# Kernel tuning notes

Hardware: AMD Instinct MI355X
Metric: run time of the kernel (lower is better)

## Reference

```python
import jax, jax.numpy as jnp
import numpy as np

N = 50000      # num nodes
E = 600000     # num edges (avg degree 12)
IN = 256       # in_feats
H = 128        # h_feats
P = 2          # prop_step
LN_EPS = 1e-5


def setup_inputs() -> dict:
    key = jax.random.key(0)
    ks = jax.random.split(key, 8)
    return {
        "in_feat": jax.random.normal(ks[0], (N, IN), jnp.float32),
        "row": jax.random.randint(ks[1], (E,), 0, N),  # target node of each edge
        "col": jax.random.randint(ks[2], (E,), 0, N),  # source node of each edge
        "lin_w": jax.random.normal(ks[3], (H, IN), jnp.float32) / np.sqrt(IN).astype(np.float32),
        "lin_b": jnp.zeros((H,), jnp.float32),
        "conv_w": jax.random.normal(ks[4], (H, H), jnp.float32) / np.sqrt(H).astype(np.float32),
        "conv_b": jnp.zeros((H,), jnp.float32),
        "root_emb": jax.random.normal(ks[5], (1, H), jnp.float32) * 0.02,
        "ln_gamma": jnp.ones((P, H), jnp.float32),
        "ln_beta": jnp.zeros((P, H), jnp.float32),
    }


def _layernorm(x, g, b):
    mu = jnp.mean(x, axis=-1, keepdims=True)
    var = jnp.mean(jnp.square(x - mu), axis=-1, keepdims=True)
    return (x - mu) * jax.lax.rsqrt(var + LN_EPS) * g + b


def reference(in_feat, row, col, lin_w, lin_b, conv_w, conv_b, root_emb, ln_gamma, ln_beta):
    n = in_feat.shape[0]
    h = in_feat @ lin_w.T + lin_b                      # [N, H]

    # OGB-style degree norm with +1 trick (original edges, row = target)
    deg = jax.ops.segment_sum(jnp.ones_like(row, dtype=h.dtype), row, num_segments=n) + 1.0
    deg_inv = 1.0 / deg                                # deg >= 1, never inf

    # GCNConv symmetric norm with self loops: D^-1/2 (A+I) D^-1/2
    loop = jnp.arange(n)
    r2 = jnp.concatenate([row, loop])                  # [E+N] targets
    c2 = jnp.concatenate([col, loop])                  # [E+N] sources
    d2 = jax.ops.segment_sum(jnp.ones_like(r2, dtype=h.dtype), r2, num_segments=n)
    dis = jnp.where(d2 > 0, jax.lax.rsqrt(jnp.maximum(d2, 1.0)), 0.0)
    ew = dis[r2] * dis[c2]                             # [E+N] edge weights

    root = root_emb[0]                                 # [H]
    ori = h
    for i in range(P):
        if i != 0:
            h = h + ori                                # residual
            h = _layernorm(h, ln_gamma[i], ln_beta[i])
            h = jax.nn.relu(h)
            # dropout=0.0 -> identity
        xw = h @ conv_w.T                              # [N, H]
        h_msg = jax.ops.segment_sum(ew[:, None] * xw[c2], r2, num_segments=n) + conv_b
        root_contrib = jax.nn.relu(h + root) * deg_inv[:, None]
        h = h_msg + root_contrib
    return h
```

## Files before the change

### kernel.cpp

```cpp
#include <hip/hip_runtime.h>

#define NN 50000
#define EE 600000
#define INF 256
#define HF 128
#define CEB ((EE + 255) / 256)

typedef __attribute__((ext_vector_type(8))) short short8;
typedef __attribute__((ext_vector_type(4))) float floatx4;

__device__ __forceinline__ unsigned short f32_to_bf16_rne(float x) {
    unsigned int u = __float_as_uint(x);
    unsigned int r = (u + 0x7FFFu + ((u >> 16) & 1u)) >> 16;
    return (unsigned short)r;
}
__device__ __forceinline__ float bf16_to_f32(unsigned short h) {
    return __uint_as_float(((unsigned int)h) << 16);
}
__device__ __forceinline__ float bf16lo_u32(unsigned int u) {
    return __uint_as_float(u << 16);
}
__device__ __forceinline__ float bf16hi_u32(unsigned int u) {
    return __uint_as_float(u & 0xFFFF0000u);
}
__device__ __forceinline__ void cvt_hilo8(float4 v0, float4 v1, short8& hs, short8& ls) {
    float x[8] = {v0.x, v0.y, v0.z, v0.w, v1.x, v1.y, v1.z, v1.w};
    union { short8 s; unsigned short u[8]; } H, L;
#pragma unroll
    for (int k = 0; k < 8; ++k) {
        unsigned short hi = f32_to_bf16_rne(x[k]);
        H.u[k] = hi;
        L.u[k] = f32_to_bf16_rne(x[k] - bf16_to_f32(hi));
    }
    hs = H.s;
    ls = L.s;
}

__global__ void count_and_prepack(const int* __restrict__ row, int* __restrict__ cnt,
                                  int* __restrict__ pos, int E,
                                  const float* __restrict__ lw, const float* __restrict__ cw,
                                  unsigned short* __restrict__ fl, unsigned short* __restrict__ fc) {
    int b = blockIdx.x;
    if (b < CEB) {
        int e = b * 256 + threadIdx.x;
        if (e < E) pos[e] = atomicAdd(&cnt[row[e]], 1);
        return;
    }
    int idx = (b - CEB) * 256 + threadIdx.x;
    const float* src;
    unsigned short* dst;
    int K, c;
    if (idx < 8192) {
        src = lw; dst = fl; K = INF; c = idx;
    } else if (idx < 12288) {
        src = cw; dst = fc; K = HF; c = idx - 8192;
    } else return;
    int lane = c & 63;
    int nt = (c >> 6) & 7;
    int hl = (c >> 9) & 1;
    int kc = c >> 10;
    int rw = nt * 16 + (lane & 15);
    int koff = kc * 32 + (lane >> 4) * 8;
    const float* p = &src[(size_t)rw * K + koff];
    float4 v0 = *reinterpret_cast<const float4*>(p);
    float4 v1 = *reinterpret_cast<const float4*>(p + 4);
    short8 hs, ls;
    cvt_hilo8(v0, v1, hs, ls);
    *reinterpret_cast<short8*>(&dst[(size_t)c * 8]) = hl ? ls : hs;
}

__global__ void scan_phase1(const int* __restrict__ cnt, int* __restrict__ bsum, int n) {
    __shared__ int sdata[256];
    int t = threadIdx.x;
    int i = blockIdx.x * 256 + t;
    sdata[t] = (i < n) ? cnt[i] : 0;
    __syncthreads();
    for (int s = 128; s > 0; s >>= 1) {
        if (t < s) sdata[t] += sdata[t + s];
        __syncthreads();
    }
    if (t == 0) bsum[blockIdx.x] = sdata[0];
}

__global__ void scan_phase3(const int* __restrict__ cnt, const int* __restrict__ bsum,
                            int* __restrict__ row_start,
                            float* __restrict__ deg_inv, float* __restrict__ dis,
                            int n, int nb, int E) {
    __shared__ int sb[256];
    __shared__ int sdata[256];
    int t = threadIdx.x;
    sb[t] = (t < nb) ? bsum[t] : 0;
    __syncthreads();
    for (int s = 1; s < 256; s <<= 1) {
        int add = (t >= s) ? sb[t - s] : 0;
        __syncthreads();
        sb[t] += add;
        __syncthreads();
    }
    int base = sb[blockIdx.x] - bsum[blockIdx.x];
    int i = blockIdx.x * 256 + t;
    int v = (i < n) ? cnt[i] : 0;
    sdata[t] = v;
    __syncthreads();
    for (int s = 1; s < 256; s <<= 1) {
        int add = (t >= s) ? sdata[t - s] : 0;
        __syncthreads();
        sdata[t] += add;
        __syncthreads();
    }
    if (i < n) {
        int ex = base + sdata[t] - v;
        row_start[i] = ex;
        float d = (float)(v + 1);
        deg_inv[i] = 1.0f / d;
        dis[i] = rsqrtf(d);
    }
    if (blockIdx.x == 0 && t == 0) row_start[n] = E;
}

__global__ void fill_csr(const int* __restrict__ row, const int* __restrict__ col,
                         const int* __restrict__ row_start, const int* __restrict__ pos,
                         int* __restrict__ csr_col, int E) {
    int e = blockIdx.x * blockDim.x + threadIdx.x;
    if (e < E) {
        int p = row_start[row[e]] + pos[e];
        __builtin_nontemporal_store(col[e], &csr_col[p]);
    }
}

template <int K, int MODE>
__global__ __launch_bounds__(256) void gemm_ldsw(
    const float* __restrict__ Af,
    const unsigned short* __restrict__ Ahg, const unsigned short* __restrict__ Alg,
    const unsigned short* __restrict__ Wf,
    const float* __restrict__ bias,
    float* __restrict__ C, unsigned short* __restrict__ Cbf,
    const float* __restrict__ h, const float* __restrict__ deg_inv,
    const float* __restrict__ dis, const float* __restrict__ root,
    const float* __restrict__ gamma, const float* __restrict__ beta,
    int M) {
    constexpr int NKC = K / 32;
    __shared__ unsigned short WS[2 * 8192];

    const int t = threadIdx.x;
    const int wave = t >> 6;
    const int lane = t & 63;
    const int lrow = lane & 15;
    const int quad = lane >> 4;
    const int bm = blockIdx.x * 64;
    int arow = bm + wave * 16 + lrow;
    if (arow >= M) arow = M - 1;

    floatx4 acc[8];
#pragma unroll
    for (int nt = 0; nt < 8; ++nt) acc[nt] = (floatx4){0.f, 0.f, 0.f, 0.f};

#pragma unroll
    for (int p = 0; p < NKC / 2; ++p) {
        if (p) __syncthreads();
        {
            const uint4* src = reinterpret_cast<const uint4*>(Wf + (size_t)p * 16384);
            uint4* dstl = reinterpret_cast<uint4*>(WS);
#pragma unroll
            for (int i = 0; i < 8; ++i) dstl[t + 256 * i] = src[t + 256 * i];
        }
        __syncthreads();
#pragma unroll
        for (int k2 = 0; k2 < 2; ++k2) {
            int kc = p * 2 + k2;
            short8 afh, afl;
            if (MODE == 0) {
                const float* ap = &Af[(size_t)arow * K + kc * 32 + quad * 8];
                float4 a0 = *reinterpret_cast<const float4*>(ap);
                float4 a1 = *reinterpret_cast<const float4*>(ap + 4);
                cvt_hilo8(a0, a1, afh, afl);
            } else {
                size_t ao = (size_t)arow * K + kc * 32 + quad * 8;
                afh = *reinterpret_cast<const short8*>(&Ahg[ao]);
                afl = *reinterpret_cast<const short8*>(&Alg[ao]);
            }
            const unsigned short* wb = &WS[k2 * 8192 + lane * 8];
#pragma unroll
            for (int nt = 0; nt < 8; ++nt) {
                short8 bfh = *reinterpret_cast<const short8*>(wb + nt * 512);
                short8 bfl = *reinterpret_cast<const short8*>(wb + 4096 + nt * 512);
                acc[nt] = __builtin_amdgcn_mfma_f32_16x16x32_bf16(afh, bfh, acc[nt], 0, 0, 0);
                acc[nt] = __builtin_amdgcn_mfma_f32_16x16x32_bf16(afl, bfh, acc[nt], 0, 0, 0);
                acc[nt] = __builtin_amdgcn_mfma_f32_16x16x32_bf16(afh, bfl, acc[nt], 0, 0, 0);
            }
        }
    }

    float cb[8], rt[8], gm[8], bt[8];
#pragma unroll
    for (int nt = 0; nt < 8; ++nt) {
        int colh = nt * 16 + lrow;
        cb[nt] = bias[colh];
        if (MODE >= 1) rt[nt] = root[colh];
        if (MODE == 1) { gm[nt] = gamma[colh]; bt[nt] = beta[colh]; }
    }

#pragma unroll
    for (int r = 0; r < 4; ++r) {
        int grow = bm + wave * 16 + quad * 4 + r;
        bool ok = (grow < M);
        int gr = ok ? grow : M - 1;
        float x[8];
        if (MODE == 0) {
#pragma unroll
            for (int nt = 0; nt < 8; ++nt) x[nt] = acc[nt][r] + cb[nt];
        } else {
            float di = deg_inv[gr];
            float hv[8];
#pragma unroll
            for (int nt = 0; nt < 8; ++nt) hv[nt] = h[(size_t)gr * HF + nt * 16 + lrow];
#pragma unroll
            for (int nt = 0; nt < 8; ++nt) {
                float v = acc[nt][r] + cb[nt] + fmaxf(hv[nt] + rt[nt], 0.f) * di;
                x[nt] = (MODE == 1) ? v + hv[nt] : v;
            }
        }
        if (MODE == 1) {
            float s = 0.f;
#pragma unroll
            for (int nt = 0; nt < 8; ++nt) s += x[nt];
#pragma unroll
            for (int m = 1; m < 16; m <<= 1) s += __shfl_xor(s, m, 64);
            float mu = s * (1.0f / HF);
            float var = 0.f;
#pragma unroll
            for (int nt = 0; nt < 8; ++nt) { float d = x[nt] - mu; var += d * d; }
#pragma unroll
            for (int m = 1; m < 16; m <<= 1) var += __shfl_xor(var, m, 64);
            float rs = rsqrtf(var * (1.0f / HF) + 1e-5f);
            float ds = dis[gr];
            if (ok) {
#pragma unroll
                for (int nt = 0; nt < 8; ++nt) {
                    int colh = nt * 16 + lrow;
                    float y = fmaxf((x[nt] - mu) * rs * gm[nt] + bt[nt], 0.f);
                    C[(size_t)grow * HF + colh] = y;
                    Cbf[(size_t)grow * HF + colh] = f32_to_bf16_rne(ds * y);
                }
            }
        } else if (MODE == 0) {
            if (ok) {
                float ds = dis[grow];
#pragma unroll
                for (int nt = 0; nt < 8; ++nt) {
                    int colh = nt * 16 + lrow;
                    C[(size_t)grow * HF + colh] = x[nt];
                    Cbf[(size_t)grow * HF + colh] = f32_to_bf16_rne(ds * x[nt]);
                }
            }
        } else {
            if (ok) {
#pragma unroll
                for (int nt = 0; nt < 8; ++nt)
                    C[(size_t)grow * HF + nt * 16 + lrow] = x[nt];
            }
        }
    }
}

__global__ void aggregate(const int* __restrict__ row_start, const int* __restrict__ csr_col,
                          const float* __restrict__ dis, const float* __restrict__ deg_inv,
                          const float* __restrict__ h, const unsigned short* __restrict__ hbf,
                          unsigned short* __restrict__ agg_hi, unsigned short* __restrict__ agg_lo,
                          int n) {
    int wid = (blockIdx.x * blockDim.x + threadIdx.x) >> 6;
    int lane = threadIdx.x & 63;
    if (wid >= n) return;
    int q = lane >> 4;
    int l16 = lane & 15;
    int s = row_start[wid];
    int e = row_start[wid + 1];
    float a0 = 0.f, a1 = 0.f, a2 = 0.f, a3 = 0.f, a4 = 0.f, a5 = 0.f, a6 = 0.f, a7 = 0.f;
    if (e - s <= 16) {
        int j0 = s + q;
        bool p0 = j0 < e, p1 = j0 + 4 < e, p2 = j0 + 8 < e, p3 = j0 + 12 < e;
        int c0 = p0 ? csr_col[j0] : 0;
        int c1 = p1 ? csr_col[j0 + 4] : 0;
        int c2 = p2 ? csr_col[j0 + 8] : 0;
        int c3 = p3 ? csr_col[j0 + 12] : 0;
        uint4 z = make_uint4(0, 0, 0, 0);
        uint4 g0 = z, g1 = z, g2 = z, g3 = z;
        if (p0) g0 = *reinterpret_cast<const uint4*>(&hbf[(size_t)c0 * HF + l16 * 8]);
        if (p1) g1 = *reinterpret_cast<const uint4*>(&hbf[(size_t)c1 * HF + l16 * 8]);
        if (p2) g2 = *reinterpret_cast<const uint4*>(&hbf[(size_t)c2 * HF + l16 * 8]);
        if (p3) g3 = *reinterpret_cast<const uint4*>(&hbf[(size_t)c3 * HF + l16 * 8]);
        a0 = bf16lo_u32(g0.x) + bf16lo_u32(g1.x) + bf16lo_u32(g2.x) + bf16lo_u32(g3.x);
        a1 = bf16hi_u32(g0.x) + bf16hi_u32(g1.x) + bf16hi_u32(g2.x) + bf16hi_u32(g3.x);
        a2 = bf16lo_u32(g0.y) + bf16lo_u32(g1.y) + bf16lo_u32(g2.y) + bf16lo_u32(g3.y);
        a3 = bf16hi_u32(g0.y) + bf16hi_u32(g1.y) + bf16hi_u32(g2.y) + bf16hi_u32(g3.y);
        a4 = bf16lo_u32(g0.z) + bf16lo_u32(g1.z) + bf16lo_u32(g2.z) + bf16lo_u32(g3.z);
        a5 = bf16hi_u32(g0.z) + bf16hi_u32(g1.z) + bf16hi_u32(g2.z) + bf16hi_u32(g3.z);
        a6 = bf16lo_u32(g0.w) + bf16lo_u32(g1.w) + bf16lo_u32(g2.w) + bf16lo_u32(g3.w);
        a7 = bf16hi_u32(g0.w) + bf16hi_u32(g1.w) + bf16hi_u32(g2.w) + bf16hi_u32(g3.w);
    } else {
        float b0 = 0.f, b1 = 0.f, b2 = 0.f, b3 = 0.f, b4 = 0.f, b5 = 0.f, b6 = 0.f, b7 = 0.f;
        int j = s + q;
        for (; j + 4 < e; j += 8) {
            int c0 = csr_col[j];
            int c1 = csr_col[j + 4];
            uint4 h0 = *reinterpret_cast<const uint4*>(&hbf[(size_t)c0 * HF + l16 * 8]);
            uint4 h1 = *reinterpret_cast<const uint4*>(&hbf[(size_t)c1 * HF + l16 * 8]);
            a0 += bf16lo_u32(h0.x); a1 += bf16hi_u32(h0.x);
            a2 += bf16lo_u32(h0.y); a3 += bf16hi_u32(h0.y);
            a4 += bf16lo_u32(h0.z); a5 += bf16hi_u32(h0.z);
            a6 += bf16lo_u32(h0.w); a7 += bf16hi_u32(h0.w);
            b0 += bf16lo_u32(h1.x); b1 += bf16hi_u32(h1.x);
            b2 += bf16lo_u32(h1.y); b3 += bf16hi_u32(h1.y);
            b4 += bf16lo_u32(h1.z); b5 += bf16hi_u32(h1.z);
            b6 += bf16lo_u32(h1.w); b7 += bf16hi_u32(h1.w);
        }
        if (j < e) {
            int c0 = csr_col[j];
            uint4 h0 = *reinterpret_cast<const uint4*>(&hbf[(size_t)c0 * HF + l16 * 8]);
            a0 += bf16lo_u32(h0.x); a1 += bf16hi_u32(h0.x);
            a2 += bf16lo_u32(h0.y); a3 += bf16hi_u32(h0.y);
            a4 += bf16lo_u32(h0.z); a5 += bf16hi_u32(h0.z);
            a6 += bf16lo_u32(h0.w); a7 += bf16hi_u32(h0.w);
        }
        a0 += b0; a1 += b1; a2 += b2; a3 += b3;
        a4 += b4; a5 += b5; a6 += b6; a7 += b7;
    }
#pragma unroll
    for (int m = 16; m < 64; m <<= 1) {
        a0 += __shfl_xor(a0, m, 64);
        a1 += __shfl_xor(a1, m, 64);
        a2 += __shfl_xor(a2, m, 64);
        a3 += __shfl_xor(a3, m, 64);
        a4 += __shfl_xor(a4, m, 64);
        a5 += __shfl_xor(a5, m, 64);
        a6 += __shfl_xor(a6, m, 64);
        a7 += __shfl_xor(a7, m, 64);
    }
    if (q == 0) {
        float dn = dis[wid];
        float di = deg_inv[wid];
        float4 hA = *reinterpret_cast<const float4*>(&h[(size_t)wid * HF + l16 * 8]);
        float4 hB = *reinterpret_cast<const float4*>(&h[(size_t)wid * HF + l16 * 8 + 4]);
        float o[8];
        o[0] = fmaf(dn, a0, di * hA.x);
        o[1] = fmaf(dn, a1, di * hA.y);
        o[2] = fmaf(dn, a2, di * hA.z);
        o[3] = fmaf(dn, a3, di * hA.w);
        o[4] = fmaf(dn, a4, di * hB.x);
        o[5] = fmaf(dn, a5, di * hB.y);
        o[6] = fmaf(dn, a6, di * hB.z);
        o[7] = fmaf(dn, a7, di * hB.w);
        unsigned short hi[8], lo[8];
#pragma unroll
        for (int k = 0; k < 8; ++k) {
            hi[k] = f32_to_bf16_rne(o[k]);
            lo[k] = f32_to_bf16_rne(o[k] - bf16_to_f32(hi[k]));
        }
        uint4 hp, lp;
        hp.x = (unsigned)hi[0] | ((unsigned)hi[1] << 16);
        hp.y = (unsigned)hi[2] | ((unsigned)hi[3] << 16);
        hp.z = (unsigned)hi[4] | ((unsigned)hi[5] << 16);
        hp.w = (unsigned)hi[6] | ((unsigned)hi[7] << 16);
        lp.x = (unsigned)lo[0] | ((unsigned)lo[1] << 16);
        lp.y = (unsigned)lo[2] | ((unsigned)lo[3] << 16);
        lp.z = (unsigned)lo[4] | ((unsigned)lo[5] << 16);
        lp.w = (unsigned)lo[6] | ((unsigned)lo[7] << 16);
        *reinterpret_cast<uint4*>(&agg_hi[(size_t)wid * HF + l16 * 8]) = hp;
        *reinterpret_cast<uint4*>(&agg_lo[(size_t)wid * HF + l16 * 8]) = lp;
    }
}

extern "C" void kernel_launch(void* const* d_in, const int* in_sizes, int n_in,
                              void* d_out, int out_size, void* d_ws, size_t ws_size,
                              hipStream_t stream) {
    const int N = NN, E = EE;
    const float* in_feat = (const float*)d_in[0];
    const int* row = (const int*)d_in[1];
    const int* col = (const int*)d_in[2];
    const float* lin_w = (const float*)d_in[3];
    const float* lin_b = (const float*)d_in[4];
    const float* conv_w = (const float*)d_in[5];
    const float* conv_b = (const float*)d_in[6];
    const float* root_emb = (const float*)d_in[7];
    const float* ln_gamma = (const float*)d_in[8];
    const float* ln_beta = (const float*)d_in[9];
    float* out = (float*)d_out;

    float* ws = (float*)d_ws;
    size_t o = 0;
    float* deg_inv = ws + o; o += N;
    float* dis = ws + o; o += N;
    int* cnt = (int*)(ws + o); o += N;
    int* row_start = (int*)(ws + o); o += N + 4;
    int* pos = (int*)(ws + o); o += E;
    int* bsum = (int*)(ws + o); o += 256;
    int* csr_col = (int*)(ws + o); o += E;
    o = (o + 3) & ~(size_t)3;
    unsigned short* fl = (unsigned short*)(ws + o); o += 32768;
    unsigned short* fc = (unsigned short*)(ws + o); o += 16384;
    float* h0 = ws + o; o += (size_t)N * HF;
    unsigned short* hbf = (unsigned short*)(ws + o); o += (size_t)N * HF / 2;
    unsigned short* agg_hi = (unsigned short*)(ws + o); o += (size_t)N * HF / 2;
    unsigned short* agg_lo = (unsigned short*)(ws + o); o += (size_t)N * HF / 2;

    const int NB = (N + 255) / 256;

    hipMemsetAsync(cnt, 0, N * sizeof(int), stream);
    count_and_prepack<<<CEB + 48, 256, 0, stream>>>(row, cnt, pos, E, lin_w, conv_w, fl, fc);
    scan_phase1<<<NB, 256, 0, stream>>>(cnt, bsum, N);
    scan_phase3<<<NB, 256, 0, stream>>>(cnt, bsum, row_start, deg_inv, dis, N, NB, E);
    fill_csr<<<CEB, 256, 0, stream>>>(row, col, row_start, pos, csr_col, E);

    const int GB = (N + 63) / 64;
    const int WB = (N + 3) / 4;

    gemm_ldsw<INF, 0><<<GB, 256, 0, stream>>>(in_feat, nullptr, nullptr, fl, lin_b,
                                              h0, hbf, nullptr, nullptr, dis, nullptr,
                                              nullptr, nullptr, N);

    aggregate<<<WB, 256, 0, stream>>>(row_start, csr_col, dis, deg_inv, h0, hbf,
                                      agg_hi, agg_lo, N);
    gemm_ldsw<HF, 1><<<GB, 256, 0, stream>>>(nullptr, agg_hi, agg_lo, fc, conv_b,
                                             h0, hbf, h0, deg_inv, dis, root_emb,
                                             ln_gamma + HF, ln_beta + HF, N);

    aggregate<<<WB, 256, 0, stream>>>(row_start, csr_col, dis, deg_inv, h0, hbf,
                                      agg_hi, agg_lo, N);
    gemm_ldsw<HF, 2><<<GB, 256, 0, stream>>>(nullptr, agg_hi, agg_lo, fc, conv_b,
                                             out, nullptr, h0, deg_inv, dis, root_emb,
                                             nullptr, nullptr, N);
}
```

Measured before the change: 292.6 us.

## Split bf16 gather table into column halves and fuse CSR fill into GEMM

Stores the scaled bf16 feature table as two 64-column halves and runs the neighbour aggregation twice, once per half. This shrinks each pass's random-gather working set to improve cache hit rates. The CSR fill kernel is folded into the first GEMM launch as extra blocks, removing a launch and letting it overlap. The trade-off is doubled aggregate launches, re-reading the CSR indices, and narrower per-lane loads.

```diff
diff --git a/kernel.cpp b/kernel.cpp
--- a/kernel.cpp
+++ b/kernel.cpp
@@ -5,6 +5,7 @@
 #define INF 256
 #define HF 128
 #define CEB ((EE + 255) / 256)
+#define GBK ((NN + 63) / 64)
 
 typedef __attribute__((ext_vector_type(8))) short short8;
 typedef __attribute__((ext_vector_type(4))) float floatx4;
@@ -118,29 +119,32 @@
     if (blockIdx.x == 0 && t == 0) row_start[n] = E;
 }
 
-__global__ void fill_csr(const int* __restrict__ row, const int* __restrict__ col,
-                         const int* __restrict__ row_start, const int* __restrict__ pos,
-                         int* __restrict__ csr_col, int E) {
-    int e = blockIdx.x * blockDim.x + threadIdx.x;
-    if (e < E) {
-        int p = row_start[row[e]] + pos[e];
-        __builtin_nontemporal_store(col[e], &csr_col[p]);
-    }
-}
-
-template <int K, int MODE>
+template <int K, int MODE, bool FILL>
 __global__ __launch_bounds__(256) void gemm_ldsw(
     const float* __restrict__ Af,
     const unsigned short* __restrict__ Ahg, const unsigned short* __restrict__ Alg,
     const unsigned short* __restrict__ Wf,
     const float* __restrict__ bias,
-    float* __restrict__ C, unsigned short* __restrict__ Cbf,
+    float* __restrict__ C,
+    unsigned short* __restrict__ hbfA, unsigned short* __restrict__ hbfB,
     const float* __restrict__ h, const float* __restrict__ deg_inv,
     const float* __restrict__ dis, const float* __restrict__ root,
     const float* __restrict__ gamma, const float* __restrict__ beta,
-    int M) {
+    int M,
+    const int* __restrict__ erow, const int* __restrict__ ecol,
+    const int* __restrict__ row_start, const int* __restrict__ pos,
+    int* __restrict__ csr_col, int E) {
     constexpr int NKC = K / 32;
     __shared__ unsigned short WS[2 * 8192];
+
+    if (FILL && blockIdx.x >= GBK) {
+        int e = (blockIdx.x - GBK) * 256 + threadIdx.x;
+        if (e < E) {
+            int p = row_start[erow[e]] + pos[e];
+            __builtin_nontemporal_store(ecol[e], &csr_col[p]);
+        }
+        return;
+    }
 
     const int t = threadIdx.x;
     const int wave = t >> 6;
@@ -240,7 +244,8 @@
                     int colh = nt * 16 + lrow;
                     float y = fmaxf((x[nt] - mu) * rs * gm[nt] + bt[nt], 0.f);
                     C[(size_t)grow * HF + colh] = y;
-                    Cbf[(size_t)grow * HF + colh] = f32_to_bf16_rne(ds * y);
+                    unsigned short* half = (nt < 4) ? hbfA : hbfB;
+                    half[(size_t)grow * 64 + (nt & 3) * 16 + lrow] = f32_to_bf16_rne(ds * y);
                 }
             }
         } else if (MODE == 0) {
@@ -250,7 +255,8 @@
                 for (int nt = 0; nt < 8; ++nt) {
                     int colh = nt * 16 + lrow;
                     C[(size_t)grow * HF + colh] = x[nt];
-                    Cbf[(size_t)grow * HF + colh] = f32_to_bf16_rne(ds * x[nt]);
+                    unsigned short* half = (nt < 4) ? hbfA : hbfB;
+                    half[(size_t)grow * 64 + (nt & 3) * 16 + lrow] = f32_to_bf16_rne(ds * x[nt]);
                 }
             }
         } else {
@@ -263,11 +269,12 @@
     }
 }
 
-__global__ void aggregate(const int* __restrict__ row_start, const int* __restrict__ csr_col,
-                          const float* __restrict__ dis, const float* __restrict__ deg_inv,
-                          const float* __restrict__ h, const unsigned short* __restrict__ hbf,
-                          unsigned short* __restrict__ agg_hi, unsigned short* __restrict__ agg_lo,
-                          int n) {
+template <int PASS>
+__global__ void aggregate_half(const int* __restrict__ row_start, const int* __restrict__ csr_col,
+                               const float* __restrict__ dis, const float* __restrict__ deg_inv,
+                               const float* __restrict__ h, const unsigned short* __restrict__ hbfH,
+                               unsigned short* __restrict__ agg_hi, unsigned short* __restrict__ agg_lo,
+                               int n) {
     int wid = (blockIdx.x * blockDim.x + threadIdx.x) >> 6;
     int lane = threadIdx.x & 63;
     if (wid >= n) return;
@@ -275,7 +282,7 @@
     int l16 = lane & 15;
     int s = row_start[wid];
     int e = row_start[wid + 1];
-    float a0 = 0.f, a1 = 0.f, a2 = 0.f, a3 = 0.f, a4 = 0.f, a5 = 0.f, a6 = 0.f, a7 = 0.f;
+    float a0 = 0.f, a1 = 0.f, a2 = 0.f, a3 = 0.f;
     if (e - s <= 16) {
         int j0 = s + q;
         bool p0 = j0 < e, p1 = j0 + 4 < e, p2 = j0 + 8 < e, p3 = j0 + 12 < e;
@@ -283,47 +290,36 @@
         int c1 = p1 ? csr_col[j0 + 4] : 0;
         int c2 = p2 ? csr_col[j0 + 8] : 0;
         int c3 = p3 ? csr_col[j0 + 12] : 0;
-        uint4 z = make_uint4(0, 0, 0, 0);
-        uint4 g0 = z, g1 = z, g2 = z, g3 = z;
-        if (p0) g0 = *reinterpret_cast<const uint4*>(&hbf[(size_t)c0 * HF + l16 * 8]);
-        if (p1) g1 = *reinterpret_cast<const uint4*>(&hbf[(size_t)c1 * HF + l16 * 8]);
-        if (p2) g2 = *reinterpret_cast<const uint4*>(&hbf[(size_t)c2 * HF + l16 * 8]);
-        if (p3) g3 = *reinterpret_cast<const uint4*>(&hbf[(size_t)c3 * HF + l16 * 8]);
+        uint2 z = make_uint2(0, 0);
+        uint2 g0 = z, g1 = z, g2 = z, g3 = z;
+        if (p0) g0 = *reinterpret_cast<const uint2*>(&hbfH[(size_t)c0 * 64 + l16 * 4]);
+        if (p1) g1 = *reinterpret_cast<const uint2*>(&hbfH[(size_t)c1 * 64 + l16 * 4]);
+        if (p2) g2 = *reinterpret_cast<const uint2*>(&hbfH[(size_t)c2 * 64 + l16 * 4]);
+        if (p3) g3 = *reinterpret_cast<const uint2*>(&hbfH[(size_t)c3 * 64 + l16 * 4]);
         a0 = bf16lo_u32(g0.x) + bf16lo_u32(g1.x) + bf16lo_u32(g2.x) + bf16lo_u32(g3.x);
         a1 = bf16hi_u32(g0.x) + bf16hi_u32(g1.x) + bf16hi_u32(g2.x) + bf16hi_u32(g3.x);
         a2 = bf16lo_u32(g0.y) + bf16lo_u32(g1.y) + bf16lo_u32(g2.y) + bf16lo_u32(g3.y);
         a3 = bf16hi_u32(g0.y) + bf16hi_u32(g1.y) + bf16hi_u32(g2.y) + bf16hi_u32(g3.y);
-        a4 = bf16lo_u32(g0.z) + bf16lo_u32(g1.z) + bf16lo_u32(g2.z) + bf16lo_u32(g3.z);
-        a5 = bf16hi_u32(g0.z) + bf16hi_u32(g1.z) + bf16hi_u32(g2.z) + bf16hi_u32(g3.z);
-        a6 = bf16lo_u32(g0.w) + bf16lo_u32(g1.w) + bf16lo_u32(g2.w) + bf16lo_u32(g3.w);
-        a7 = bf16hi_u32(g0.w) + bf16hi_u32(g1.w) + bf16hi_u32(g2.w) + bf16hi_u32(g3.w);
     } else {
-        float b0 = 0.f, b1 = 0.f, b2 = 0.f, b3 = 0.f, b4 = 0.f, b5 = 0.f, b6 = 0.f, b7 = 0.f;
+        float b0 = 0.f, b1 = 0.f, b2 = 0.f, b3 = 0.f;
         int j = s + q;
         for (; j + 4 < e; j += 8) {
             int c0 = csr_col[j];
             int c1 = csr_col[j + 4];
-            uint4 h0 = *reinterpret_cast<const uint4*>(&hbf[(size_t)c0 * HF + l16 * 8]);
-            uint4 h1 = *reinterpret_cast<const uint4*>(&hbf[(size_t)c1 * HF + l16 * 8]);
-            a0 += bf16lo_u32(h0.x); a1 += bf16hi_u32(h0.x);
-            a2 += bf16lo_u32(h0.y); a3 += bf16hi_u32(h0.y);
-            a4 += bf16lo_u32(h0.z); a5 += bf16hi_u32(h0.z);
-            a6 += bf16lo_u32(h0.w); a7 += bf16hi_u32(h0.w);
-            b0 += bf16lo_u32(h1.x); b1 += bf16hi_u32(h1.x);
-            b2 += bf16lo_u32(h1.y); b3 += bf16hi_u32(h1.y);
-            b4 += bf16lo_u32(h1.z); b5 += bf16hi_u32(h1.z);
-            b6 += bf16lo_u32(h1.w); b7 += bf16hi_u32(h1.w);
+            uint2 g0 = *reinterpret_cast<const uint2*>(&hbfH[(size_t)c0 * 64 + l16 * 4]);
+            uint2 g1 = *reinterpret_cast<const uint2*>(&hbfH[(size_t)c1 * 64 + l16 * 4]);
+            a0 += bf16lo_u32(g0.x); a1 += bf16hi_u32(g0.x);
+            a2 += bf16lo_u32(g0.y); a3 += bf16hi_u32(g0.y);
+            b0 += bf16lo_u32(g1.x); b1 += bf16hi_u32(g1.x);
+            b2 += bf16lo_u32(g1.y); b3 += bf16hi_u32(g1.y);
         }
         if (j < e) {
             int c0 = csr_col[j];
-            uint4 h0 = *reinterpret_cast<const uint4*>(&hbf[(size_t)c0 * HF + l16 * 8]);
-            a0 += bf16lo_u32(h0.x); a1 += bf16hi_u32(h0.x);
-            a2 += bf16lo_u32(h0.y); a3 += bf16hi_u32(h0.y);
-            a4 += bf16lo_u32(h0.z); a5 += bf16hi_u32(h0.z);
-            a6 += bf16lo_u32(h0.w); a7 += bf16hi_u32(h0.w);
+            uint2 g0 = *reinterpret_cast<const uint2*>(&hbfH[(size_t)c0 * 64 + l16 * 4]);
+            a0 += bf16lo_u32(g0.x); a1 += bf16hi_u32(g0.x);
+            a2 += bf16lo_u32(g0.y); a3 += bf16hi_u32(g0.y);
         }
         a0 += b0; a1 += b1; a2 += b2; a3 += b3;
-        a4 += b4; a5 += b5; a6 += b6; a7 += b7;
     }
 #pragma unroll
     for (int m = 16; m < 64; m <<= 1) {
@@ -331,42 +327,27 @@
         a1 += __shfl_xor(a1, m, 64);
         a2 += __shfl_xor(a2, m, 64);
         a3 += __shfl_xor(a3, m, 64);
-        a4 += __shfl_xor(a4, m, 64);
-        a5 += __shfl_xor(a5, m, 64);
-        a6 += __shfl_xor(a6, m, 64);
-        a7 += __shfl_xor(a7, m, 64);
     }
     if (q == 0) {
         float dn = dis[wid];
         float di = deg_inv[wid];
-        float4 hA = *reinterpret_cast<const float4*>(&h[(size_t)wid * HF + l16 * 8]);
-        float4 hB = *reinterpret_cast<const float4*>(&h[(size_t)wid * HF + l16 * 8 + 4]);
-        float o[8];
-        o[0] = fmaf(dn, a0, di * hA.x);
-        o[1] = fmaf(dn, a1, di * hA.y);
-        o[2] = fmaf(dn, a2, di * hA.z);
-        o[3] = fmaf(dn, a3, di * hA.w);
-        o[4] = fmaf(dn, a4, di * hB.x);
-        o[5] = fmaf(dn, a5, di * hB.y);
-        o[6] = fmaf(dn, a6, di * hB.z);
-        o[7] = fmaf(dn, a7, di * hB.w);
-        unsigned short hi[8], lo[8];
-#pragma unroll
-        for (int k = 0; k < 8; ++k) {
-            hi[k] = f32_to_bf16_rne(o[k]);
-            lo[k] = f32_to_bf16_rne(o[k] - bf16_to_f32(hi[k]));
-        }
-        uint4 hp, lp;
-        hp.x = (unsigned)hi[0] | ((unsigned)hi[1] << 16);
-        hp.y = (unsigned)hi[2] | ((unsigned)hi[3] << 16);
-        hp.z = (unsigned)hi[4] | ((unsigned)hi[5] << 16);
-        hp.w = (unsigned)hi[6] | ((unsigned)hi[7] << 16);
-        lp.x = (unsigned)lo[0] | ((unsigned)lo[1] << 16);
-        lp.y = (unsigned)lo[2] | ((unsigned)lo[3] << 16);
-        lp.z = (unsigned)lo[4] | ((unsigned)lo[5] << 16);
-        lp.w = (unsigned)lo[6] | ((unsigned)lo[7] << 16);
-        *reinterpret_cast<uint4*>(&agg_hi[(size_t)wid * HF + l16 * 8]) = hp;
-        *reinterpret_cast<uint4*>(&agg_lo[(size_t)wid * HF + l16 * 8]) = lp;
+        float4 hv = *reinterpret_cast<const float4*>(&h[(size_t)wid * HF + PASS * 64 + l16 * 4]);
+        float o[4];
+        o[0] = fmaf(dn, a0, di * hv.x);
+        o[1] = fmaf(dn, a1, di * hv.y);
+        o[2] = fmaf(dn, a2, di * hv.z);
+        o[3] = fmaf(dn, a3, di * hv.w);
+        ushort4 hp, lp;
+        unsigned short* hpp = &hp.x;
+        unsigned short* lpp = &lp.x;
+#pragma unroll
+        for (int k = 0; k < 4; ++k) {
+            unsigned short hi = f32_to_bf16_rne(o[k]);
+            hpp[k] = hi;
+            lpp[k] = f32_to_bf16_rne(o[k] - bf16_to_f32(hi));
+        }
+        *reinterpret_cast<ushort4*>(&agg_hi[(size_t)wid * HF + PASS * 64 + l16 * 4]) = hp;
+        *reinterpret_cast<ushort4*>(&agg_lo[(size_t)wid * HF + PASS * 64 + l16 * 4]) = lp;
     }
 }
 
@@ -399,7 +380,8 @@
     unsigned short* fl = (unsigned short*)(ws + o); o += 32768;
     unsigned short* fc = (unsigned short*)(ws + o); o += 16384;
     float* h0 = ws + o; o += (size_t)N * HF;
-    unsigned short* hbf = (unsigned short*)(ws + o); o += (size_t)N * HF / 2;
+    unsigned short* hbfA = (unsigned short*)(ws + o); o += (size_t)N * 32;
+    unsigned short* hbfB = (unsigned short*)(ws + o); o += (size_t)N * 32;
     unsigned short* agg_hi = (unsigned short*)(ws + o); o += (size_t)N * HF / 2;
     unsigned short* agg_lo = (unsigned short*)(ws + o); o += (size_t)N * HF / 2;
 
@@ -409,24 +391,29 @@
     count_and_prepack<<<CEB + 48, 256, 0, stream>>>(row, cnt, pos, E, lin_w, conv_w, fl, fc);
     scan_phase1<<<NB, 256, 0, stream>>>(cnt, bsum, N);
     scan_phase3<<<NB, 256, 0, stream>>>(cnt, bsum, row_start, deg_inv, dis, N, NB, E);
-    fill_csr<<<CEB, 256, 0, stream>>>(row, col, row_start, pos, csr_col, E);
-
-    const int GB = (N + 63) / 64;
+
     const int WB = (N + 3) / 4;
 
-    gemm_ldsw<INF, 0><<<GB, 256, 0, stream>>>(in_feat, nullptr, nullptr, fl, lin_b,
-                                              h0, hbf, nullptr, nullptr, dis, nullptr,
-                                              nullptr, nullptr, N);
-
-    aggregate<<<WB, 256, 0, stream>>>(row_start, csr_col, dis, deg_inv, h0, hbf,
-                                      agg_hi, agg_lo, N);
-    gemm_ldsw<HF, 1><<<GB, 256, 0, stream>>>(nullptr, agg_hi, agg_lo, fc, conv_b,
-                                             h0, hbf, h0, deg_inv, dis, root_emb,
-                                             ln_gamma + HF, ln_beta + HF, N);
-
-    aggregate<<<WB, 256, 0, stream>>>(row_start, csr_col, dis, deg_inv, h0, hbf,
-                                      agg_hi, agg_lo, N);
-    gemm_ldsw<HF, 2><<<GB, 256, 0, stream>>>(nullptr, agg_hi, agg_lo, fc, conv_b,
-                                             out, nullptr, h0, deg_inv, dis, root_emb,
-                                             nullptr, nullptr, N);
-}
+    gemm_ldsw<INF, 0, true><<<GBK + CEB, 256, 0, stream>>>(
+        in_feat, nullptr, nullptr, fl, lin_b, h0, hbfA, hbfB,
+        nullptr, nullptr, dis, nullptr, nullptr, nullptr, N,
+        row, col, row_start, pos, csr_col, E);
+
+    aggregate_half<0><<<WB, 256, 0, stream>>>(row_start, csr_col, dis, deg_inv, h0, hbfA,
+                                              agg_hi, agg_lo, N);
+    aggregate_half<1><<<WB, 256, 0, stream>>>(row_start, csr_col, dis, deg_inv, h0, hbfB,
+                                              agg_hi, agg_lo, N);
+    gemm_ldsw<HF, 1, false><<<GBK, 256, 0, stream>>>(
+        nullptr, agg_hi, agg_lo, fc, conv_b, h0, hbfA, hbfB,
+        h0, deg_inv, dis, root_emb, ln_gamma + HF, ln_beta + HF, N,
+        nullptr, nullptr, nullptr, nullptr, nullptr, 0);
+
+    aggregate_half<0><<<WB, 256, 0, stream>>>(row_start, csr_col, dis, deg_inv, h0, hbfA,
+                                              agg_hi, agg_lo, N);
+    aggregate_half<1><<<WB, 256, 0, stream>>>(row_start, csr_col, dis, deg_inv, h0, hbfB,
+                                              agg_hi, agg_lo, N);
+    gemm_ldsw<HF, 2, false><<<GBK, 256, 0, stream>>>(
+        nullptr, agg_hi, agg_lo, fc, conv_b, out, nullptr, nullptr,
+        h0, deg_inv, dis, root_emb, nullptr, nullptr, N,
+        nullptr, nullptr, nullptr, nullptr, nullptr, 0);
+}
```

Measured after the change: 313.0 us. 1.07x slower.
